# Kernel tuning notes

Hardware: AMD Instinct MI355X
Metric: run time of the kernel (lower is better)

## Reference

```python
import jax, jax.numpy as jnp
import numpy as np
import math

NEG_INF = -1000000000.0
D_EMBED = 1024
D_K = 1024
N_HEADS = 16
D_H = D_EMBED // N_HEADS


def setup_inputs() -> dict:
    key = jax.random.key(0)
    ks = jax.random.split(key, 12)
    B, S = 2, 2048
    s = 0.02
    return {
        "embed": jax.random.normal(ks[0], (B, S, D_EMBED), dtype=jnp.float32),
        "key": jax.random.normal(ks[1], (B, S, D_K), dtype=jnp.float32),
        "attn_mask": jax.random.randint(ks[2], (B, S, S), 0, 2, dtype=jnp.int32),
        "Wq": jax.random.normal(ks[3], (D_EMBED, D_EMBED), dtype=jnp.float32) * s,
        "bq": jnp.zeros((D_EMBED,), dtype=jnp.float32),
        "Wk": jax.random.normal(ks[4], (D_EMBED, D_K), dtype=jnp.float32) * s,
        "bk": jnp.zeros((D_EMBED,), dtype=jnp.float32),
        "Wv": jax.random.normal(ks[5], (D_EMBED, D_K), dtype=jnp.float32) * s,
        "bv": jnp.zeros((D_EMBED,), dtype=jnp.float32),
        "Wo": jax.random.normal(ks[6], (D_EMBED, D_EMBED), dtype=jnp.float32) * s,
        "bo": jnp.zeros((D_EMBED,), dtype=jnp.float32),
    }


def _alibi_bias(seq_len: int, n_heads: int) -> jnp.ndarray:
    # symmetric |i-j| distances, slopes 2^-(8k/H) for k=1..H
    r = jnp.arange(seq_len)
    pos = jnp.abs(r[None, :] - r[:, None]).astype(jnp.float32)  # [S, S]
    step = 8.0 / n_heads
    ms = 2.0 ** (-jnp.arange(step, 8.0 + step, step, dtype=jnp.float32))  # [H]
    return ms[:, None, None] * pos[None, :, :]  # [H, S, S]


def reference(embed, key, attn_mask, Wq, bq, Wk, bk, Wv, bv, Wo, bo):
    B, Sq, _ = embed.shape
    Sk = key.shape[1]
    Q = embed @ Wq.T + bq          # [B, Sq, D]
    K = key @ Wk.T + bk            # [B, Sk, D]
    V = key @ Wv.T + bv            # [B, Sk, D]
    Qh = Q.reshape(B, Sq, N_HEADS, D_H).transpose(0, 2, 1, 3)  # [B, H, Sq, d_h]
    Kh = K.reshape(B, Sk, N_HEADS, D_H).transpose(0, 2, 1, 3)
    Vh = V.reshape(B, Sk, N_HEADS, D_H).transpose(0, 2, 1, 3)
    attn = jnp.einsum("bhqd,bhkd->bhqk", Qh, Kh)
    # ALiBi bias subtracted BEFORE scaling (as in source)
    attn = attn - _alibi_bias(Sq, N_HEADS)[None]
    attn = attn * (1.0 / math.sqrt(D_EMBED))  # note: scale uses d_embed, not d_h
    attn = jnp.where(attn_mask[:, None, :, :] == 0, NEG_INF, attn)
    attn = jax.nn.softmax(attn, axis=-1)
    out = jnp.einsum("bhqk,bhkd->bhqd", attn, Vh)
    out = out.transpose(0, 2, 1, 3).reshape(B, Sq, D_EMBED)
    return out @ Wo.T + bo
```

## Files before the change

kernel.cpp:

```cpp
#include <hip/hip_runtime.h>


typedef _Float16 f16;
typedef __attribute__((ext_vector_type(8))) _Float16 f16x8;
typedef __attribute__((ext_vector_type(4))) _Float16 f16x4;
typedef __attribute__((ext_vector_type(4))) float f32x4;
typedef unsigned long long u64;
typedef unsigned int u32;

#define MFMA16 __builtin_amdgcn_mfma_f32_16x16x32_f16

__global__ __launch_bounds__(256) void k_convert(
    const float* __restrict__ embed, const float* __restrict__ key,
    const float* __restrict__ wq, const float* __restrict__ wk,
    const float* __restrict__ wv, const float* __restrict__ wo,
    f16* __restrict__ xe, f16* __restrict__ xk,
    f16* __restrict__ wqh, f16* __restrict__ wkh,
    f16* __restrict__ wvh, f16* __restrict__ woh)
{
    long g = (long)blockIdx.x * 256 + threadIdx.x;
    const float* src; f16* dst; long off;
    if (g < 524288)       { src = embed; dst = xe; off = g; }
    else if (g < 1048576) { src = key;   dst = xk; off = g - 524288; }
    else {
        long t = g - 1048576; int wi = (int)(t >> 17); off = t & 131071;
        if (wi == 0)      { src = wq; dst = wqh; }
        else if (wi == 1) { src = wk; dst = wkh; }
        else if (wi == 2) { src = wv; dst = wvh; }
        else              { src = wo; dst = woh; }
    }
    const float4* s4 = (const float4*)src;
    float4 a = s4[off * 2], b = s4[off * 2 + 1];
    f16x8 o;
    o[0]=(f16)a.x; o[1]=(f16)a.y; o[2]=(f16)a.z; o[3]=(f16)a.w;
    o[4]=(f16)b.x; o[5]=(f16)b.y; o[6]=(f16)b.z; o[7]=(f16)b.w;
    *(f16x8*)(dst + off * 8) = o;
}

__global__ __launch_bounds__(256) void k_packmask(
    const int* __restrict__ mask, u64* __restrict__ bits)
{
    int gw = (blockIdx.x * 256 + threadIdx.x) >> 6;
    int lane = threadIdx.x & 63;
    const int* row = mask + (long)gw * 2048;
    u64* out = bits + (long)gw * 32;
    #pragma unroll 4
    for (int c = 0; c < 32; ++c) {
        int v = row[c * 64 + lane];
        u64 b = __ballot(v != 0);
        if (lane == 0) out[c] = b;
    }
}

__global__ __launch_bounds__(256) void k_qkv(
    const f16* __restrict__ xe, const f16* __restrict__ xk,
    const f16* __restrict__ wqh, const f16* __restrict__ wkh, const f16* __restrict__ wvh,
    const float* __restrict__ bq, const float* __restrict__ bk, const float* __restrict__ bv,
    f16* __restrict__ Qh, f16* __restrict__ Kh, f16* __restrict__ Vt)
{
    int bid = blockIdx.x;
    int which = bid >> 8;
    int rr_ = bid & 255;
    int tm = rr_ >> 3, tn = rr_ & 7;
    const f16* X = (which == 0) ? xe : xk;
    const f16* W = (which == 0) ? wqh : (which == 1) ? wkh : wvh;
    const float* bias = (which == 0) ? bq : (which == 1) ? bk : bv;

    __shared__ f16 smem[128 * 136];
    f16* la = smem;
    f16* lb = smem + 128 * 64;

    int tid = threadIdx.x;
    int lane = tid & 63, wid = tid >> 6;
    int wr = wid >> 1, wc = wid & 1;
    int lm = lane & 15, qd = lane >> 4;

    f32x4 acc[4][4];
    #pragma unroll
    for (int i = 0; i < 4; i++)
        #pragma unroll
        for (int j = 0; j < 4; j++) acc[i][j] = (f32x4)0.0f;

    int m0 = tm * 128, n0 = tn * 128;

    for (int kt = 0; kt < 16; ++kt) {
        int k0 = kt * 64;
        __syncthreads();
        #pragma unroll
        for (int t = 0; t < 4; ++t) {
            int cid = tid + t * 256;
            int row = cid >> 3;
            int cg = cid & 7;
            int sw = cg ^ (row & 7);
            *(f16x8*)&la[row * 64 + sw * 8] =
                *(const f16x8*)&X[(long)(m0 + row) * 1024 + k0 + cg * 8];
            *(f16x8*)&lb[row * 64 + sw * 8] =
                *(const f16x8*)&W[(long)(n0 + row) * 1024 + k0 + cg * 8];
        }
        __syncthreads();
        #pragma unroll
        for (int ks = 0; ks < 2; ++ks) {
            f16x8 af[4], bfr[4];
            #pragma unroll
            for (int i = 0; i < 4; i++) {
                int m = 64 * wr + 16 * i + lm;
                int g = (ks * 4 + qd) ^ (m & 7);
                af[i] = *(const f16x8*)&la[m * 64 + g * 8];
                int n = 64 * wc + 16 * i + lm;
                int g2 = (ks * 4 + qd) ^ (n & 7);
                bfr[i] = *(const f16x8*)&lb[n * 64 + g2 * 8];
            }
            #pragma unroll
            for (int i = 0; i < 4; i++)
                #pragma unroll
                for (int j = 0; j < 4; j++)
                    acc[i][j] = MFMA16(af[i], bfr[j], acc[i][j], 0, 0, 0);
        }
    }

    if (which == 2) {
        #pragma unroll
        for (int j = 0; j < 4; j++) {
            int n = n0 + 64 * wc + 16 * j + lm;
            float bb = bias[n];
            int h = n >> 6, d = n & 63;
            #pragma unroll
            for (int i = 0; i < 4; i++) {
                int mbase = m0 + 64 * wr + 16 * i + 4 * qd;
                f16x4 pk;
                #pragma unroll
                for (int r = 0; r < 4; ++r) pk[r] = (f16)(acc[i][j][r] + bb);
                int b = mbase >> 11, s = mbase & 2047;
                *(f16x4*)&Vt[(((long)(b * 16 + h)) * 64 + d) * 2048 + s] = pk;
            }
        }
    } else {
        f16* dst = (which == 0) ? Qh : Kh;
        __syncthreads();
        #pragma unroll
        for (int j = 0; j < 4; j++) {
            int col = 64 * wc + 16 * j + lm;
            float bb = bias[n0 + col];
            #pragma unroll
            for (int i = 0; i < 4; i++) {
                int row = 64 * wr + 16 * i + 4 * qd;
                #pragma unroll
                for (int r = 0; r < 4; ++r)
                    smem[(row + r) * 136 + col] = (f16)(acc[i][j][r] + bb);
            }
        }
        __syncthreads();
        #pragma unroll
        for (int t = 0; t < 8; ++t) {
            int ci = tid + t * 256;
            int row = ci >> 4, cg = ci & 15;
            f16x8 v = *(const f16x8*)&smem[row * 136 + cg * 8];
            int m = m0 + row;
            int b = m >> 11, s = m & 2047;
            int h = (n0 >> 6) + (cg >> 3);
            int d0 = (cg & 7) * 8;
            *(f16x8*)&dst[(((long)(b * 16 + h)) * 2048 + s) * 64 + d0] = v;
        }
    }
}

__global__ __launch_bounds__(512, 4) void k_attn(
    const f16* __restrict__ Qh, const f16* __restrict__ Kh, const f16* __restrict__ Vt,
    const u64* __restrict__ mbits, f16* __restrict__ O)
{
    int bid = blockIdx.x;
    int qt = bid & 15;
    int h = (bid >> 4) & 15;
    int b = bid >> 8;
    int q0 = qt * 128;

    const f16* Qg = Qh + ((long)(b * 16 + h)) * 2048 * 64;
    const f16* Kg = Kh + ((long)(b * 16 + h)) * 2048 * 64;
    const f16* Vg = Vt + ((long)(b * 16 + h)) * 64 * 2048;

    __shared__ f16 ks[128 * 64];
    __shared__ f16 vs[64 * 128];
    __shared__ f16 ps[8][16 * 128];

    int tid = threadIdx.x, lane = tid & 63, wid = tid >> 6;
    int lm = lane & 15, qd = lane >> 4;

    int qrow = q0 + 16 * wid + lm;
    const u64* Mrow = mbits + ((long)(b * 2048) + qrow) * 32;

    f16x8 aq[2];
    #pragma unroll
    for (int ksi = 0; ksi < 2; ++ksi)
        aq[ksi] = *(const f16x8*)&Qg[(long)qrow * 64 + ksi * 32 + qd * 8];

    f32x4 oacc[4], lacc;
    #pragma unroll
    for (int c = 0; c < 4; c++) oacc[c] = (f32x4)0.0f;
    lacc = (f32x4)0.0f;
    f16x8 vone;
    #pragma unroll
    for (int j = 0; j < 8; j++) vone[j] = (f16)1.0f;

    const float c1 = 0.0450842252f;
    float negc2 = -__builtin_amdgcn_exp2f(-0.5f * (float)(h + 1)) * c1;
    const float c3 = 5.7707801634f;

    for (int kt = 0; kt < 16; ++kt) {
        int k0 = kt * 128;
        __syncthreads();
        #pragma unroll
        for (int t = 0; t < 2; ++t) {
            int cid = tid + t * 512;
            int row = cid >> 3, cg = cid & 7;
            int sw = cg ^ (row & 7);
            *(f16x8*)&ks[row * 64 + sw * 8] =
                *(const f16x8*)&Kg[(long)(k0 + row) * 64 + cg * 8];
            int vrow = cid >> 4, vg = cid & 15;
            int vsw = vg ^ (vrow & 7);
            *(f16x8*)&vs[vrow * 128 + vsw * 8] =
                *(const f16x8*)&Vg[(long)vrow * 2048 + k0 + vg * 8];
        }
        __syncthreads();

        u64 w0 = Mrow[kt * 2], w1 = Mrow[kt * 2 + 1];

        f32x4 sacc[8];
        #pragma unroll
        for (int c = 0; c < 8; c++) sacc[c] = (f32x4)0.0f;
        #pragma unroll
        for (int ksi = 0; ksi < 2; ++ksi) {
            #pragma unroll
            for (int c = 0; c < 8; c++) {
                int kr = 16 * c + lm;
                int g = (ksi * 4 + qd) ^ (kr & 7);
                f16x8 ak = *(const f16x8*)&ks[kr * 64 + g * 8];
                sacc[c] = MFMA16(ak, aq[ksi], sacc[c], 0, 0, 0);
            }
        }

        float qmkb = (float)(qrow - k0 - 4 * qd);
        int shb = 4 * qd;
        #pragma unroll
        for (int c = 0; c < 8; c++) {
            u32 nib = (u32)(((c < 4) ? w0 : w1) >> (16 * (c & 3) + shb)) & 15u;
            float qmkc = qmkb - 16.0f * (float)c;
            float p[4];
            #pragma unroll
            for (int r = 0; r < 4; ++r) {
                float t2 = fmaf(sacc[c][r], c1, -c3);
                float dd = qmkc - (float)r;
                float u = fmaf(fabsf(dd), negc2, t2);
                u = ((nib >> r) & 1u) ? u : -1e30f;
                p[r] = __builtin_amdgcn_exp2f(u);
            }
            f16x4 pk;
            #pragma unroll
            for (int r = 0; r < 4; ++r) pk[r] = (f16)p[r];
            int g8 = (2 * c + (qd >> 1)) ^ (lm & 7);
            *(f16x4*)&ps[wid][lm * 128 + g8 * 8 + (qd & 1) * 4] = pk;
        }

        #pragma unroll
        for (int k4 = 0; k4 < 4; ++k4) {
            int gp = (k4 * 4 + qd) ^ (lm & 7);
            f16x8 pa = *(const f16x8*)&ps[wid][lm * 128 + gp * 8];
            #pragma unroll
            for (int cc = 0; cc < 4; ++cc) {
                int d = 16 * cc + lm;
                int g = (k4 * 4 + qd) ^ (d & 7);
                f16x8 vb = *(const f16x8*)&vs[d * 128 + g * 8];
                oacc[cc] = MFMA16(pa, vb, oacc[cc], 0, 0, 0);
            }
            lacc = MFMA16(pa, vone, lacc, 0, 0, 0);
        }
    }

    #pragma unroll
    for (int r = 0; r < 4; ++r) {
        float linv = 1.0f / fmaxf(lacc[r], 1e-30f);
        long rowbase = ((long)(b * 2048 + q0 + 16 * wid + 4 * qd + r)) * 1024 + h * 64;
        #pragma unroll
        for (int cc = 0; cc < 4; ++cc)
            O[rowbase + 16 * cc + lm] = (f16)(oacc[cc][r] * linv);
    }
}

__global__ __launch_bounds__(256) void k_proj(
    const f16* __restrict__ Oh, const f16* __restrict__ woh,
    const float* __restrict__ bo, float* __restrict__ out)
{
    int bid = blockIdx.x;
    int tm = bid >> 3, tn = bid & 7;

    __shared__ f16 la[128 * 64];
    __shared__ f16 lb[128 * 64];

    int tid = threadIdx.x;
    int lane = tid & 63, wid = tid >> 6;
    int wr = wid >> 1, wc = wid & 1;
    int lm = lane & 15, qd = lane >> 4;

    f32x4 acc[4][4];
    #pragma unroll
    for (int i = 0; i < 4; i++)
        #pragma unroll
        for (int j = 0; j < 4; j++) acc[i][j] = (f32x4)0.0f;

    int m0 = tm * 128, n0 = tn * 128;

    for (int kt = 0; kt < 16; ++kt) {
        int k0 = kt * 64;
        __syncthreads();
        #pragma unroll
        for (int t = 0; t < 4; ++t) {
            int cid = tid + t * 256;
            int row = cid >> 3;
            int cg = cid & 7;
            int sw = cg ^ (row & 7);
            *(f16x8*)&la[row * 64 + sw * 8] =
                *(const f16x8*)&Oh[(long)(m0 + row) * 1024 + k0 + cg * 8];
            *(f16x8*)&lb[row * 64 + sw * 8] =
                *(const f16x8*)&woh[(long)(n0 + row) * 1024 + k0 + cg * 8];
        }
        __syncthreads();
        #pragma unroll
        for (int ks = 0; ks < 2; ++ks) {
            f16x8 af[4], bfr[4];
            #pragma unroll
            for (int i = 0; i < 4; i++) {
                int m = 64 * wr + 16 * i + lm;
                int g = (ks * 4 + qd) ^ (m & 7);
                af[i] = *(const f16x8*)&la[m * 64 + g * 8];
                int n = 64 * wc + 16 * i + lm;
                int g2 = (ks * 4 + qd) ^ (n & 7);
                bfr[i] = *(const f16x8*)&lb[n * 64 + g2 * 8];
            }
            #pragma unroll
            for (int i = 0; i < 4; i++)
                #pragma unroll
                for (int j = 0; j < 4; j++)
                    acc[i][j] = MFMA16(af[i], bfr[j], acc[i][j], 0, 0, 0);
        }
    }

    #pragma unroll
    for (int j = 0; j < 4; j++) {
        int n = n0 + 64 * wc + 16 * j + lm;
        float bb = bo[n];
        #pragma unroll
        for (int i = 0; i < 4; i++) {
            int mbase = m0 + 64 * wr + 16 * i + 4 * qd;
            #pragma unroll
            for (int r = 0; r < 4; ++r)
                out[(long)(mbase + r) * 1024 + n] = acc[i][j][r] + bb;
        }
    }
}

extern "C" void kernel_launch(void* const* d_in, const int* in_sizes, int n_in,
                              void* d_out, int out_size, void* d_ws, size_t ws_size,
                              hipStream_t stream)
{
    const float* embed = (const float*)d_in[0];
    const float* key   = (const float*)d_in[1];
    const int*   mask  = (const int*)d_in[2];
    const float* Wq = (const float*)d_in[3];
    const float* bq = (const float*)d_in[4];
    const float* Wk = (const float*)d_in[5];
    const float* bk = (const float*)d_in[6];
    const float* Wv = (const float*)d_in[7];
    const float* bv = (const float*)d_in[8];
    const float* Wo = (const float*)d_in[9];
    const float* bo = (const float*)d_in[10];

    char* ws = (char*)d_ws;
    f16* xe  = (f16*)(ws + 0);
    f16* xk  = (f16*)(ws + 8388608);
    f16* wqh = (f16*)(ws + 16777216);
    f16* wkh = (f16*)(ws + 18874368);
    f16* wvh = (f16*)(ws + 20971520);
    f16* woh = (f16*)(ws + 23068672);
    f16* Qh  = (f16*)(ws + 25165824);
    f16* Kh  = (f16*)(ws + 33554432);
    f16* Vt  = (f16*)(ws + 41943040);
    f16* Oh  = (f16*)(ws + 50331648);
    u64* mb  = (u64*)(ws + 58720256);
    float* out = (float*)d_out;

    k_convert<<<6144, 256, 0, stream>>>(embed, key, Wq, Wk, Wv, Wo,
                                        xe, xk, wqh, wkh, wvh, woh);
    k_packmask<<<1024, 256, 0, stream>>>(mask, mb);
    k_qkv<<<768, 256, 0, stream>>>(xe, xk, wqh, wkh, wvh, bq, bk, bv, Qh, Kh, Vt);
    k_attn<<<512, 512, 0, stream>>>(Qh, Kh, Vt, mb, Oh);
    k_proj<<<256, 256, 0, stream>>>(Oh, woh, bo, out);
}
```

Baseline: 275.5 us.

## Fuse conversions into GEMM loads, split attention over keys, merge partials in projection

Drops the standalone fp32-to-fp16 conversion and mask-packing kernels. The QKV GEMM now converts fp32 inputs and weights while loading tiles, and extra blocks in the same launch pack the mask. The output projection converts Wo the same way. Attention is split into two key halves to double the grid. Each half writes unnormalized fp32 partial outputs and row sums, and the projection sums the halves and normalizes them while loading its A tile. The probability tile is processed in 32-key chunks with a smaller LDS buffer, and the occupancy hint is raised. The trade-off is more fp32 traffic: the fp32 inputs and weights are re-read for every GEMM tile, and the fp32 partial buffers are larger than the old fp16 output.

```diff
diff --git a/kernel.cpp b/kernel.cpp
--- a/kernel.cpp
+++ b/kernel.cpp
@@ -10,67 +10,44 @@
 
 #define MFMA16 __builtin_amdgcn_mfma_f32_16x16x32_f16
 
-__global__ __launch_bounds__(256) void k_convert(
-    const float* __restrict__ embed, const float* __restrict__ key,
+__global__ __launch_bounds__(256) void k_qkvm(
+    const float* __restrict__ embed, const float* __restrict__ keyf,
+    const int* __restrict__ mask,
     const float* __restrict__ wq, const float* __restrict__ wk,
-    const float* __restrict__ wv, const float* __restrict__ wo,
-    f16* __restrict__ xe, f16* __restrict__ xk,
-    f16* __restrict__ wqh, f16* __restrict__ wkh,
-    f16* __restrict__ wvh, f16* __restrict__ woh)
-{
-    long g = (long)blockIdx.x * 256 + threadIdx.x;
-    const float* src; f16* dst; long off;
-    if (g < 524288)       { src = embed; dst = xe; off = g; }
-    else if (g < 1048576) { src = key;   dst = xk; off = g - 524288; }
-    else {
-        long t = g - 1048576; int wi = (int)(t >> 17); off = t & 131071;
-        if (wi == 0)      { src = wq; dst = wqh; }
-        else if (wi == 1) { src = wk; dst = wkh; }
-        else if (wi == 2) { src = wv; dst = wvh; }
-        else              { src = wo; dst = woh; }
-    }
-    const float4* s4 = (const float4*)src;
-    float4 a = s4[off * 2], b = s4[off * 2 + 1];
-    f16x8 o;
-    o[0]=(f16)a.x; o[1]=(f16)a.y; o[2]=(f16)a.z; o[3]=(f16)a.w;
-    o[4]=(f16)b.x; o[5]=(f16)b.y; o[6]=(f16)b.z; o[7]=(f16)b.w;
-    *(f16x8*)(dst + off * 8) = o;
-}
-
-__global__ __launch_bounds__(256) void k_packmask(
-    const int* __restrict__ mask, u64* __restrict__ bits)
-{
-    int gw = (blockIdx.x * 256 + threadIdx.x) >> 6;
-    int lane = threadIdx.x & 63;
-    const int* row = mask + (long)gw * 2048;
-    u64* out = bits + (long)gw * 32;
-    #pragma unroll 4
-    for (int c = 0; c < 32; ++c) {
-        int v = row[c * 64 + lane];
-        u64 b = __ballot(v != 0);
-        if (lane == 0) out[c] = b;
-    }
-}
-
-__global__ __launch_bounds__(256) void k_qkv(
-    const f16* __restrict__ xe, const f16* __restrict__ xk,
-    const f16* __restrict__ wqh, const f16* __restrict__ wkh, const f16* __restrict__ wvh,
-    const float* __restrict__ bq, const float* __restrict__ bk, const float* __restrict__ bv,
-    f16* __restrict__ Qh, f16* __restrict__ Kh, f16* __restrict__ Vt)
+    const float* __restrict__ wv,
+    const float* __restrict__ bq, const float* __restrict__ bk,
+    const float* __restrict__ bv,
+    f16* __restrict__ Qh, f16* __restrict__ Kh, f16* __restrict__ Vt,
+    u64* __restrict__ bits)
 {
     int bid = blockIdx.x;
+    int tid = threadIdx.x;
+
+    if (bid >= 768) {
+        int gw = (bid - 768) * 4 + (tid >> 6);
+        int lane = tid & 63;
+        const int* row = mask + (long)gw * 2048;
+        u64* outb = bits + (long)gw * 32;
+        #pragma unroll 4
+        for (int c = 0; c < 32; ++c) {
+            int v = row[c * 64 + lane];
+            u64 bm = __ballot(v != 0);
+            if (lane == 0) outb[c] = bm;
+        }
+        return;
+    }
+
     int which = bid >> 8;
     int rr_ = bid & 255;
     int tm = rr_ >> 3, tn = rr_ & 7;
-    const f16* X = (which == 0) ? xe : xk;
-    const f16* W = (which == 0) ? wqh : (which == 1) ? wkh : wvh;
+    const float* Xf = (which == 0) ? embed : keyf;
+    const float* Wf = (which == 0) ? wq : (which == 1) ? wk : wv;
     const float* bias = (which == 0) ? bq : (which == 1) ? bk : bv;
 
     __shared__ f16 smem[128 * 136];
     f16* la = smem;
     f16* lb = smem + 128 * 64;
 
-    int tid = threadIdx.x;
     int lane = tid & 63, wid = tid >> 6;
     int wr = wid >> 1, wc = wid & 1;
     int lm = lane & 15, qd = lane >> 4;
@@ -92,10 +69,22 @@
             int row = cid >> 3;
             int cg = cid & 7;
             int sw = cg ^ (row & 7);
-            *(f16x8*)&la[row * 64 + sw * 8] =
-                *(const f16x8*)&X[(long)(m0 + row) * 1024 + k0 + cg * 8];
-            *(f16x8*)&lb[row * 64 + sw * 8] =
-                *(const f16x8*)&W[(long)(n0 + row) * 1024 + k0 + cg * 8];
+            {
+                const float4* s4 = (const float4*)&Xf[(long)(m0 + row) * 1024 + k0 + cg * 8];
+                float4 a = s4[0], b2 = s4[1];
+                f16x8 o;
+                o[0]=(f16)a.x; o[1]=(f16)a.y; o[2]=(f16)a.z; o[3]=(f16)a.w;
+                o[4]=(f16)b2.x; o[5]=(f16)b2.y; o[6]=(f16)b2.z; o[7]=(f16)b2.w;
+                *(f16x8*)&la[row * 64 + sw * 8] = o;
+            }
+            {
+                const float4* s4 = (const float4*)&Wf[(long)(n0 + row) * 1024 + k0 + cg * 8];
+                float4 a = s4[0], b2 = s4[1];
+                f16x8 o;
+                o[0]=(f16)a.x; o[1]=(f16)a.y; o[2]=(f16)a.z; o[3]=(f16)a.w;
+                o[4]=(f16)b2.x; o[5]=(f16)b2.y; o[6]=(f16)b2.z; o[7]=(f16)b2.w;
+                *(f16x8*)&lb[row * 64 + sw * 8] = o;
+            }
         }
         __syncthreads();
         #pragma unroll
@@ -164,14 +153,15 @@
     }
 }
 
-__global__ __launch_bounds__(512, 4) void k_attn(
+__global__ __launch_bounds__(512, 8) void k_attn(
     const f16* __restrict__ Qh, const f16* __restrict__ Kh, const f16* __restrict__ Vt,
-    const u64* __restrict__ mbits, f16* __restrict__ O)
+    const u64* __restrict__ mbits, float* __restrict__ On, float* __restrict__ lsum)
 {
     int bid = blockIdx.x;
     int qt = bid & 15;
     int h = (bid >> 4) & 15;
-    int b = bid >> 8;
+    int b = (bid >> 8) & 1;
+    int half = bid >> 9;
     int q0 = qt * 128;
 
     const f16* Qg = Qh + ((long)(b * 16 + h)) * 2048 * 64;
@@ -180,7 +170,7 @@
 
     __shared__ f16 ks[128 * 64];
     __shared__ f16 vs[64 * 128];
-    __shared__ f16 ps[8][16 * 128];
+    __shared__ f16 ps[8][16 * 32];
 
     int tid = threadIdx.x, lane = tid & 63, wid = tid >> 6;
     int lm = lane & 15, qd = lane >> 4;
@@ -205,7 +195,9 @@
     float negc2 = -__builtin_amdgcn_exp2f(-0.5f * (float)(h + 1)) * c1;
     const float c3 = 5.7707801634f;
 
-    for (int kt = 0; kt < 16; ++kt) {
+    int kt0 = half * 8;
+    for (int kk = 0; kk < 8; ++kk) {
+        int kt = kt0 + kk;
         int k0 = kt * 128;
         __syncthreads();
         #pragma unroll
@@ -223,71 +215,71 @@
         __syncthreads();
 
         u64 w0 = Mrow[kt * 2], w1 = Mrow[kt * 2 + 1];
-
-        f32x4 sacc[8];
-        #pragma unroll
-        for (int c = 0; c < 8; c++) sacc[c] = (f32x4)0.0f;
-        #pragma unroll
-        for (int ksi = 0; ksi < 2; ++ksi) {
-            #pragma unroll
-            for (int c = 0; c < 8; c++) {
-                int kr = 16 * c + lm;
-                int g = (ksi * 4 + qd) ^ (kr & 7);
-                f16x8 ak = *(const f16x8*)&ks[kr * 64 + g * 8];
-                sacc[c] = MFMA16(ak, aq[ksi], sacc[c], 0, 0, 0);
-            }
-        }
-
-        float qmkb = (float)(qrow - k0 - 4 * qd);
-        int shb = 4 * qd;
-        #pragma unroll
-        for (int c = 0; c < 8; c++) {
-            u32 nib = (u32)(((c < 4) ? w0 : w1) >> (16 * (c & 3) + shb)) & 15u;
-            float qmkc = qmkb - 16.0f * (float)c;
-            float p[4];
-            #pragma unroll
-            for (int r = 0; r < 4; ++r) {
-                float t2 = fmaf(sacc[c][r], c1, -c3);
-                float dd = qmkc - (float)r;
-                float u = fmaf(fabsf(dd), negc2, t2);
-                u = ((nib >> r) & 1u) ? u : -1e30f;
-                p[r] = __builtin_amdgcn_exp2f(u);
-            }
-            f16x4 pk;
-            #pragma unroll
-            for (int r = 0; r < 4; ++r) pk[r] = (f16)p[r];
-            int g8 = (2 * c + (qd >> 1)) ^ (lm & 7);
-            *(f16x4*)&ps[wid][lm * 128 + g8 * 8 + (qd & 1) * 4] = pk;
-        }
-
-        #pragma unroll
-        for (int k4 = 0; k4 < 4; ++k4) {
-            int gp = (k4 * 4 + qd) ^ (lm & 7);
-            f16x8 pa = *(const f16x8*)&ps[wid][lm * 128 + gp * 8];
-            #pragma unroll
-            for (int cc = 0; cc < 4; ++cc) {
-                int d = 16 * cc + lm;
-                int g = (k4 * 4 + qd) ^ (d & 7);
+        float qmk = (float)(qrow - k0);
+
+        #pragma unroll
+        for (int t = 0; t < 4; ++t) {
+            f32x4 sacc0 = (f32x4)0.0f, sacc1 = (f32x4)0.0f;
+            #pragma unroll
+            for (int ksi = 0; ksi < 2; ++ksi) {
+                int kr0 = 32 * t + lm;
+                int g0 = (ksi * 4 + qd) ^ (kr0 & 7);
+                f16x8 ak0 = *(const f16x8*)&ks[kr0 * 64 + g0 * 8];
+                sacc0 = MFMA16(ak0, aq[ksi], sacc0, 0, 0, 0);
+                int kr1 = 32 * t + 16 + lm;
+                int g1 = (ksi * 4 + qd) ^ (kr1 & 7);
+                f16x8 ak1 = *(const f16x8*)&ks[kr1 * 64 + g1 * 8];
+                sacc1 = MFMA16(ak1, aq[ksi], sacc1, 0, 0, 0);
+            }
+            #pragma unroll
+            for (int cc = 0; cc < 2; ++cc) {
+                const f32x4& sa = cc ? sacc1 : sacc0;
+                int c = 2 * t + cc;
+                u32 nib = (u32)(((c < 4) ? w0 : w1) >> (16 * (c & 3) + 4 * qd)) & 15u;
+                float qmkc = qmk - (float)(16 * c + 4 * qd);
+                f16x4 pk;
+                #pragma unroll
+                for (int r = 0; r < 4; ++r) {
+                    float t2 = fmaf(sa[r], c1, -c3);
+                    float u = fmaf(fabsf(qmkc - (float)r), negc2, t2);
+                    u = ((nib >> r) & 1u) ? u : -1e30f;
+                    pk[r] = (f16)__builtin_amdgcn_exp2f(u);
+                }
+                *(f16x4*)&ps[wid][lm * 32 + cc * 16 + 4 * qd] = pk;
+            }
+            f16x8 pa = *(const f16x8*)&ps[wid][lm * 32 + qd * 8];
+            #pragma unroll
+            for (int cc2 = 0; cc2 < 4; ++cc2) {
+                int d = 16 * cc2 + lm;
+                int g = (t * 4 + qd) ^ (d & 7);
                 f16x8 vb = *(const f16x8*)&vs[d * 128 + g * 8];
-                oacc[cc] = MFMA16(pa, vb, oacc[cc], 0, 0, 0);
+                oacc[cc2] = MFMA16(pa, vb, oacc[cc2], 0, 0, 0);
             }
             lacc = MFMA16(pa, vone, lacc, 0, 0, 0);
         }
     }
 
+    float* Onh = On + (long)half * 4096 * 1024;
+    float* lh = lsum + half * 65536;
+    int qloc = 16 * wid + 4 * qd;
     #pragma unroll
     for (int r = 0; r < 4; ++r) {
-        float linv = 1.0f / fmaxf(lacc[r], 1e-30f);
-        long rowbase = ((long)(b * 2048 + q0 + 16 * wid + 4 * qd + r)) * 1024 + h * 64;
+        long base = ((long)(b * 2048 + q0 + qloc + r)) * 1024 + h * 64;
         #pragma unroll
         for (int cc = 0; cc < 4; ++cc)
-            O[rowbase + 16 * cc + lm] = (f16)(oacc[cc][r] * linv);
+            Onh[base + 16 * cc + lm] = oacc[cc][r];
+    }
+    if (lm == 0) {
+        #pragma unroll
+        for (int r = 0; r < 4; ++r)
+            lh[(b * 2048 + q0 + qloc + r) * 16 + h] = lacc[r];
     }
 }
 
 __global__ __launch_bounds__(256) void k_proj(
-    const f16* __restrict__ Oh, const f16* __restrict__ woh,
-    const float* __restrict__ bo, float* __restrict__ out)
+    const float* __restrict__ On, const float* __restrict__ lsum,
+    const float* __restrict__ wo, const float* __restrict__ bo,
+    float* __restrict__ out)
 {
     int bid = blockIdx.x;
     int tm = bid >> 3, tn = bid & 7;
@@ -317,10 +309,29 @@
             int row = cid >> 3;
             int cg = cid & 7;
             int sw = cg ^ (row & 7);
-            *(f16x8*)&la[row * 64 + sw * 8] =
-                *(const f16x8*)&Oh[(long)(m0 + row) * 1024 + k0 + cg * 8];
-            *(f16x8*)&lb[row * 64 + sw * 8] =
-                *(const f16x8*)&woh[(long)(n0 + row) * 1024 + k0 + cg * 8];
+            {
+                int rg = m0 + row;
+                float l0 = lsum[rg * 16 + kt];
+                float l1 = lsum[65536 + rg * 16 + kt];
+                float lv = 1.0f / fmaxf(l0 + l1, 1e-30f);
+                const float4* p0 = (const float4*)&On[(long)rg * 1024 + k0 + cg * 8];
+                const float4* p1 = (const float4*)((const char*)p0 + 16777216);
+                float4 a0 = p0[0], a1 = p0[1], b0 = p1[0], b1 = p1[1];
+                f16x8 o;
+                o[0]=(f16)((a0.x+b0.x)*lv); o[1]=(f16)((a0.y+b0.y)*lv);
+                o[2]=(f16)((a0.z+b0.z)*lv); o[3]=(f16)((a0.w+b0.w)*lv);
+                o[4]=(f16)((a1.x+b1.x)*lv); o[5]=(f16)((a1.y+b1.y)*lv);
+                o[6]=(f16)((a1.z+b1.z)*lv); o[7]=(f16)((a1.w+b1.w)*lv);
+                *(f16x8*)&la[row * 64 + sw * 8] = o;
+            }
+            {
+                const float4* s4 = (const float4*)&wo[(long)(n0 + row) * 1024 + k0 + cg * 8];
+                float4 a = s4[0], b2 = s4[1];
+                f16x8 o;
+                o[0]=(f16)a.x; o[1]=(f16)a.y; o[2]=(f16)a.z; o[3]=(f16)a.w;
+                o[4]=(f16)b2.x; o[5]=(f16)b2.y; o[6]=(f16)b2.z; o[7]=(f16)b2.w;
+                *(f16x8*)&lb[row * 64 + sw * 8] = o;
+            }
         }
         __syncthreads();
         #pragma unroll
@@ -374,23 +385,16 @@
     const float* bo = (const float*)d_in[10];
 
     char* ws = (char*)d_ws;
-    f16* xe  = (f16*)(ws + 0);
-    f16* xk  = (f16*)(ws + 8388608);
-    f16* wqh = (f16*)(ws + 16777216);
-    f16* wkh = (f16*)(ws + 18874368);
-    f16* wvh = (f16*)(ws + 20971520);
-    f16* woh = (f16*)(ws + 23068672);
-    f16* Qh  = (f16*)(ws + 25165824);
-    f16* Kh  = (f16*)(ws + 33554432);
-    f16* Vt  = (f16*)(ws + 41943040);
-    f16* Oh  = (f16*)(ws + 50331648);
-    u64* mb  = (u64*)(ws + 58720256);
+    u64*   mb = (u64*)(ws + 0);
+    f16*   Qh = (f16*)(ws + 1048576);
+    f16*   Kh = (f16*)(ws + 9437184);
+    f16*   Vt = (f16*)(ws + 17825792);
+    float* On = (float*)(ws + 26214400);
+    float* ls = (float*)(ws + 59768832);
     float* out = (float*)d_out;
 
-    k_convert<<<6144, 256, 0, stream>>>(embed, key, Wq, Wk, Wv, Wo,
-                                        xe, xk, wqh, wkh, wvh, woh);
-    k_packmask<<<1024, 256, 0, stream>>>(mask, mb);
-    k_qkv<<<768, 256, 0, stream>>>(xe, xk, wqh, wkh, wvh, bq, bk, bv, Qh, Kh, Vt);
-    k_attn<<<512, 512, 0, stream>>>(Qh, Kh, Vt, mb, Oh);
-    k_proj<<<256, 256, 0, stream>>>(Oh, woh, bo, out);
+    k_qkvm<<<1792, 256, 0, stream>>>(embed, key, mask, Wq, Wk, Wv,
+                                     bq, bk, bv, Qh, Kh, Vt, mb);
+    k_attn<<<1024, 512, 0, stream>>>(Qh, Kh, Vt, mb, On, ls);
+    k_proj<<<256, 256, 0, stream>>>(On, ls, Wo, bo, out);
 }
```

Measured after the change: 403.8 us. +46.6%, slower.
